# Kernel optimization log

Measured on AMD Instinct MI355X. Metric: run time of the kernel, lower is better.

The kernel has to match this reference:

```python
import jax, jax.numpy as jnp
import numpy as np

WORD_THRES = 0.2
COS_EPS = 1e-8
NEG_INF = -1e9


def setup_inputs() -> dict:
    key = jax.random.key(0)
    k1, k2, k3, k4 = jax.random.split(key, 4)
    B, L, V, E, A = 1024, 256, 50000, 300, 30
    inputs = jax.random.randint(k1, (B, L), 0, V)            # token ids, 0 == pad
    w_emb = jax.random.normal(k2, (V, E), dtype=jnp.float32) * 0.1
    a_emb = jax.random.normal(k3, (A, E), dtype=jnp.float32)
    a_weight = jax.random.uniform(k4, (A,), dtype=jnp.float32)
    return {"inputs": inputs, "w_emb": w_emb, "a_emb": a_emb, "a_weight": a_weight}


def reference(inputs, w_emb, a_emb, a_weight):
    # inputs: [B, L] int ids; w_emb: [V, E]; a_emb: [A, E]; a_weight: [A]
    inputs_len = (inputs != 0).sum(axis=1).astype(jnp.float32)      # [B]
    x_wrd = w_emb[inputs]                                            # [B, L, E]

    # cosine similarity between each aspect and each word (torch semantics:
    # dot / (max(||a||, eps) * max(||x||, eps)))
    a_norm = jnp.maximum(jnp.linalg.norm(a_emb, axis=-1), COS_EPS)   # [A]
    x_norm = jnp.maximum(jnp.linalg.norm(x_wrd, axis=-1), COS_EPS)   # [B, L]
    dot = jnp.einsum("ae,ble->abl", a_emb, x_wrd)                    # [A, B, L]
    sim = dot / (a_norm[:, None, None] * x_norm[None, :, :])

    # Threshold(word_thres, 0): x if x > thres else 0, then scale by aspect weight
    sim = jnp.where(sim > WORD_THRES, sim, 0.0) * a_weight[:, None, None]

    # centroid score: relu(sim).max over aspects, summed over seq, length-normalized
    centroid = jnp.maximum(sim, 0.0).max(axis=0)                     # [B, L]
    centroid_score = centroid.sum(axis=1) / (inputs_len + 1e-5)      # [B]

    # attention: mask exact zeros to -1e9, max over aspects, softmax over seq
    sim_m = jnp.where(sim == 0.0, NEG_INF, sim)
    scores = sim_m.max(axis=0)                                       # [B, L]
    a = jax.nn.softmax(scores, axis=1)                               # [B, L]

    z = jnp.einsum("bl,ble->be", a, x_wrd)                           # [B, E]
    enc_out = z * (centroid_score > 1e-4).astype(z.dtype)[:, None]
    return enc_out, a, centroid_score
```

## Files before the change

kernel.cpp:

```cpp
#include <hip/hip_runtime.h>
#include <math.h>

#define BB 1024
#define LL 256
#define VV 50000
#define EE 300
#define AA 30
#define WORD_THRES 0.2f
#define COS_EPS_F 1e-8f
#define NEG_INF_F -1e9f
#define RECHECK_DELTA 1e-3f

typedef __attribute__((ext_vector_type(8))) short bf16x8;
typedef __attribute__((ext_vector_type(4))) float f32x4;

#define MFMA16(a, b, c) __builtin_amdgcn_mfma_f32_16x16x32_bf16((a), (b), (c), 0, 0, 0)

__device__ __forceinline__ unsigned pack_hi(float a, float b) {
    return (__float_as_uint(a) >> 16) | (__float_as_uint(b) & 0xFFFF0000u);
}
__device__ __forceinline__ float hi_part(float a) {
    return __uint_as_float(__float_as_uint(a) & 0xFFFF0000u);
}
__device__ __forceinline__ void cvt_hilo(const float4 f0, const float4 f1,
                                         uint4& uh, uint4& ul) {
    uh.x = pack_hi(f0.x, f0.y);
    uh.y = pack_hi(f0.z, f0.w);
    uh.z = pack_hi(f1.x, f1.y);
    uh.w = pack_hi(f1.z, f1.w);
    const float l0 = f0.x - hi_part(f0.x), l1 = f0.y - hi_part(f0.y);
    const float l2 = f0.z - hi_part(f0.z), l3 = f0.w - hi_part(f0.w);
    const float l4 = f1.x - hi_part(f1.x), l5 = f1.y - hi_part(f1.y);
    const float l6 = f1.z - hi_part(f1.z), l7 = f1.w - hi_part(f1.w);
    ul.x = pack_hi(l0, l1);
    ul.y = pack_hi(l2, l3);
    ul.z = pack_hi(l4, l5);
    ul.w = pack_hi(l6, l7);
}

__global__ void __launch_bounds__(256) cent_kernel(
    const float* __restrict__ w_emb,
    const float* __restrict__ a_emb,
    const float* __restrict__ a_weight,
    float* __restrict__ cent)
{
    __shared__ uint4 s_bfrag[40 * 64];
    __shared__ float s_scale[32];
    __shared__ float s_aw[32];

    const int t = threadIdx.x;
    const int l = t & 63;
    const int w = t >> 6;
    const int m = l & 15;
    const int kg = l >> 4;

    {
        const int a = t >> 3, j = t & 7;
        if (a < AA) {
            const float4* a4 = (const float4*)a_emb + a * 75;
            float n2a = 0.f;
            for (int c = j; c < 75; c += 8) {
                const float4 x = a4[c];
                n2a += x.x * x.x + x.y * x.y + x.z * x.z + x.w * x.w;
            }
            n2a += __shfl_xor(n2a, 1);
            n2a += __shfl_xor(n2a, 2);
            n2a += __shfl_xor(n2a, 4);
            if (j == 0) {
                s_scale[a] = 1.f / fmaxf(sqrtf(n2a), COS_EPS_F);
                s_aw[a] = a_weight[a];
            }
        }
        if (t == 30 || t == 31) { s_scale[t] = 0.f; s_aw[t] = 0.f; }
    }

    for (int ks = w; ks < 10; ks += 4) {
        const int kb = kg * 8 + 32 * ks;
#pragma unroll
        for (int tt = 0; tt < 2; ++tt) {
            const int col = tt * 16 + m;
            float4 f0 = {0.f, 0.f, 0.f, 0.f}, f1 = {0.f, 0.f, 0.f, 0.f};
            if (col < AA) {
                const float* ap = a_emb + col * EE;
                if (kb <= 296) f0 = *(const float4*)(ap + kb);
                if (kb <= 292) f1 = *(const float4*)(ap + kb + 4);
            }
            uint4 uh, ul;
            cvt_hilo(f0, f1, uh, ul);
            s_bfrag[(ks * 4 + tt * 2 + 0) * 64 + l] = uh;
            s_bfrag[(ks * 4 + tt * 2 + 1) * 64 + l] = ul;
        }
    }
    __syncthreads();

    const int vbase = blockIdx.x * 64 + w * 16;
    const int v = vbase + m;
    const float* __restrict__ rowp = w_emb + (size_t)((v < VV) ? v : 0) * EE;

    f32x4 acc0 = {0.f, 0.f, 0.f, 0.f};
    f32x4 acc1 = {0.f, 0.f, 0.f, 0.f};
    float n2 = 0.f;
    const uint4* __restrict__ bp0 = s_bfrag + l;

#pragma unroll 3
    for (int ks = 0; ks < 9; ++ks) {
        const int kb = kg * 8 + 32 * ks;
        const float4 f0 = *(const float4*)(rowp + kb);
        const float4 f1 = *(const float4*)(rowp + kb + 4);
        n2 = fmaf(f0.x, f0.x, fmaf(f0.y, f0.y, fmaf(f0.z, f0.z, fmaf(f0.w, f0.w, n2))));
        n2 = fmaf(f1.x, f1.x, fmaf(f1.y, f1.y, fmaf(f1.z, f1.z, fmaf(f1.w, f1.w, n2))));
        uint4 uh, ul;
        cvt_hilo(f0, f1, uh, ul);
        const bf16x8 ah = __builtin_bit_cast(bf16x8, uh);
        const bf16x8 al = __builtin_bit_cast(bf16x8, ul);
        const uint4* bp = bp0 + ks * 256;
        const bf16x8 bh0 = __builtin_bit_cast(bf16x8, bp[0]);
        const bf16x8 bl0 = __builtin_bit_cast(bf16x8, bp[64]);
        const bf16x8 bh1 = __builtin_bit_cast(bf16x8, bp[128]);
        const bf16x8 bl1 = __builtin_bit_cast(bf16x8, bp[192]);
        acc0 = MFMA16(ah, bh0, acc0);
        acc1 = MFMA16(ah, bh1, acc1);
        acc0 = MFMA16(ah, bl0, acc0);
        acc1 = MFMA16(ah, bl1, acc1);
        acc0 = MFMA16(al, bh0, acc0);
        acc1 = MFMA16(al, bh1, acc1);
    }
    {
        const int kb = kg * 8 + 288;
        float4 f0 = {0.f, 0.f, 0.f, 0.f}, f1 = {0.f, 0.f, 0.f, 0.f};
        if (kb <= 296) f0 = *(const float4*)(rowp + kb);
        if (kb <= 292) f1 = *(const float4*)(rowp + kb + 4);
        n2 = fmaf(f0.x, f0.x, fmaf(f0.y, f0.y, fmaf(f0.z, f0.z, fmaf(f0.w, f0.w, n2))));
        n2 = fmaf(f1.x, f1.x, fmaf(f1.y, f1.y, fmaf(f1.z, f1.z, fmaf(f1.w, f1.w, n2))));
        uint4 uh, ul;
        cvt_hilo(f0, f1, uh, ul);
        const bf16x8 ah = __builtin_bit_cast(bf16x8, uh);
        const bf16x8 al = __builtin_bit_cast(bf16x8, ul);
        const uint4* bp = bp0 + 9 * 256;
        const bf16x8 bh0 = __builtin_bit_cast(bf16x8, bp[0]);
        const bf16x8 bl0 = __builtin_bit_cast(bf16x8, bp[64]);
        const bf16x8 bh1 = __builtin_bit_cast(bf16x8, bp[128]);
        const bf16x8 bl1 = __builtin_bit_cast(bf16x8, bp[192]);
        acc0 = MFMA16(ah, bh0, acc0);
        acc1 = MFMA16(ah, bh1, acc1);
        acc0 = MFMA16(ah, bl0, acc0);
        acc1 = MFMA16(ah, bl1, acc1);
        acc0 = MFMA16(al, bh0, acc0);
        acc1 = MFMA16(al, bh1, acc1);
    }

    n2 += __shfl_xor(n2, 16);
    n2 += __shfl_xor(n2, 32);

    const float sc0 = s_scale[m], aw0 = s_aw[m];
    const float sc1 = s_scale[16 + m], aw1 = s_aw[16 + m];
    const bool col1ok = (16 + m) < AA;
    float mx[4];
#pragma unroll
    for (int j = 0; j < 4; ++j) {
        const int r = kg * 4 + j;
        const float n2r = __int_as_float(
            __builtin_amdgcn_ds_bpermute(r << 2, __float_as_int(n2)));
        const float inv_x = 1.f / fmaxf(sqrtf(n2r), COS_EPS_F);
        float c0 = acc0[j] * sc0 * inv_x;
        float c1 = acc1[j] * sc1 * inv_x;
        if (fabsf(c0 - WORD_THRES) < RECHECK_DELTA) {
            const int rr = vbase + r;
            const float* wr = w_emb + (size_t)((rr < VV) ? rr : 0) * EE;
            const float* ar = a_emb + m * EE;
            float d = 0.f;
            for (int k = 0; k < EE; ++k) d = fmaf(wr[k], ar[k], d);
            c0 = d * sc0 * inv_x;
        }
        if (col1ok && fabsf(c1 - WORD_THRES) < RECHECK_DELTA) {
            const int rr = vbase + r;
            const float* wr = w_emb + (size_t)((rr < VV) ? rr : 0) * EE;
            const float* ar = a_emb + (16 + m) * EE;
            float d = 0.f;
            for (int k = 0; k < EE; ++k) d = fmaf(wr[k], ar[k], d);
            c1 = d * sc1 * inv_x;
        }
        float mj = fmaxf((c0 > WORD_THRES) ? c0 * aw0 : 0.f,
                         (c1 > WORD_THRES) ? c1 * aw1 : 0.f);
        mj = fmaxf(mj, __shfl_xor(mj, 1));
        mj = fmaxf(mj, __shfl_xor(mj, 2));
        mj = fmaxf(mj, __shfl_xor(mj, 4));
        mj = fmaxf(mj, __shfl_xor(mj, 8));
        mx[j] = mj;
    }
    if (m == 0 && vbase < VV) {
        const float4 o = {mx[0], mx[1], mx[2], mx[3]};
        *(float4*)(cent + vbase + kg * 4) = o;
    }
}

__global__ void __launch_bounds__(256) row_kernel(
    const int* __restrict__ inputs,
    const float* __restrict__ w_emb,
    const float* __restrict__ cent,
    float* __restrict__ out)
{
    const int b = blockIdx.x;
    const int t = threadIdx.x;
    const int wid = t >> 6, lane = t & 63;

    __shared__ float pA[4], pB[4], pC[4], pD[4];
    __shared__ int s_nact;
    __shared__ int s_act_id[LL];
    __shared__ float s_act_w[LL];

    const int id = inputs[b * LL + t];
    const float c = cent[id];
    const float score = (c > 0.f) ? c : NEG_INF_F;
    const float cnt = (id != 0) ? 1.f : 0.f;
    if (t == 0) s_nact = 0;

    float s1 = c, s2 = cnt, s3 = score;
#pragma unroll
    for (int o = 32; o > 0; o >>= 1) {
        s1 += __shfl_down(s1, o);
        s2 += __shfl_down(s2, o);
        s3 = fmaxf(s3, __shfl_down(s3, o));
    }
    if (lane == 0) { pA[wid] = s1; pB[wid] = s2; pC[wid] = s3; }
    __syncthreads();

    const float sum_c = pA[0] + pA[1] + pA[2] + pA[3];
    const float len   = pB[0] + pB[1] + pB[2] + pB[3];
    const float mx    = fmaxf(fmaxf(pC[0], pC[1]), fmaxf(pC[2], pC[3]));

    const float p = expf(score - mx);
    float s4 = p;
#pragma unroll
    for (int o = 32; o > 0; o >>= 1) s4 += __shfl_down(s4, o);
    if (lane == 0) pD[wid] = s4;
    __syncthreads();
    const float sum_p = pD[0] + pD[1] + pD[2] + pD[3];

    const float a_l = p / sum_p;
    const float cs = sum_c / (len + 1e-5f);
    const float gate = (cs > 1e-4f) ? 1.f : 0.f;

    out[BB * EE + b * LL + t] = a_l;
    if (t == 0) out[BB * EE + BB * LL + b] = cs;

    if (score > -1e8f) {
        const int i = atomicAdd(&s_nact, 1);
        s_act_id[i] = id;
        s_act_w[i] = a_l;
    }
    __syncthreads();
    const int n = s_nact;

    if (t < EE / 4) {
        float4 acc = {0.f, 0.f, 0.f, 0.f};
        for (int i = 0; i < n; ++i) {
            const float wgt = s_act_w[i];
            const float4 r = *(const float4*)(w_emb + (size_t)s_act_id[i] * EE + 4 * t);
            acc.x += wgt * r.x; acc.y += wgt * r.y;
            acc.z += wgt * r.z; acc.w += wgt * r.w;
        }
        acc.x *= gate; acc.y *= gate; acc.z *= gate; acc.w *= gate;
        *(float4*)(out + b * EE + 4 * t) = acc;
    }
}

extern "C" void kernel_launch(void* const* d_in, const int* in_sizes, int n_in,
                              void* d_out, int out_size, void* d_ws, size_t ws_size,
                              hipStream_t stream) {
    const int* inputs = (const int*)d_in[0];
    const float* w_emb = (const float*)d_in[1];
    const float* a_emb = (const float*)d_in[2];
    const float* a_weight = (const float*)d_in[3];
    float* out = (float*)d_out;
    float* cent = (float*)d_ws;

    cent_kernel<<<(VV + 63) / 64, 256, 0, stream>>>(w_emb, a_emb, a_weight, cent);
    row_kernel<<<BB, 256, 0, stream>>>(inputs, w_emb, cent, out);
}
```

Before: 114.4 us.

## Prefetch embedding rows in registers and map one row per wavefront

In cent_kernel the K loop is fully unrolled into 10 steps. Five float4 pairs are prefetched into registers ahead of use, which hides global load latency, and the clamped loads replace the guarded tail step. row_kernel now gives each batch row to one wavefront, four rows per block, so all reductions are wave shuffles with no block barriers, and all 64 lanes take part in the weighted gather instead of 75 threads per block. The recheck delta is also tightened. This adds register pressure and leaves one launch of 256 blocks for the row stage.

```diff
diff --git a/kernel.cpp b/kernel.cpp
--- a/kernel.cpp
+++ b/kernel.cpp
@@ -9,7 +9,7 @@
 #define WORD_THRES 0.2f
 #define COS_EPS_F 1e-8f
 #define NEG_INF_F -1e9f
-#define RECHECK_DELTA 1e-3f
+#define RECHECK_DELTA 2e-4f
 
 typedef __attribute__((ext_vector_type(8))) short bf16x8;
 typedef __attribute__((ext_vector_type(4))) float f32x4;
@@ -36,6 +36,14 @@
     ul.y = pack_hi(l2, l3);
     ul.z = pack_hi(l4, l5);
     ul.w = pack_hi(l6, l7);
+}
+
+__device__ __forceinline__ void ld_pair(const float* __restrict__ rowp, int kb,
+                                        float4& a, float4& b) {
+    const int k0 = (kb > 296) ? 296 : kb;
+    const int k1 = (kb + 4 > 296) ? 296 : (kb + 4);
+    a = *(const float4*)(rowp + k0);
+    b = *(const float4*)(rowp + k1);
 }
 
 __global__ void __launch_bounds__(256) cent_kernel(
@@ -102,41 +110,29 @@
     float n2 = 0.f;
     const uint4* __restrict__ bp0 = s_bfrag + l;
 
-#pragma unroll 3
-    for (int ks = 0; ks < 9; ++ks) {
-        const int kb = kg * 8 + 32 * ks;
-        const float4 f0 = *(const float4*)(rowp + kb);
-        const float4 f1 = *(const float4*)(rowp + kb + 4);
+    float4 pa[5], pb[5];
+#pragma unroll
+    for (int i = 0; i < 5; ++i)
+        ld_pair(rowp, kg * 8 + 32 * i, pa[i], pb[i]);
+
+#pragma unroll
+    for (int i = 0; i < 10; ++i) {
+        const int s = i % 5;
+        float4 f0 = pa[s], f1 = pb[s];
+        if (i < 5)
+            ld_pair(rowp, kg * 8 + 32 * (i + 5), pa[s], pb[s]);
+        if (i == 9) {
+            const float4 z = {0.f, 0.f, 0.f, 0.f};
+            if (kg >= 2) f0 = z;
+            if (kg >= 1) f1 = z;
+        }
         n2 = fmaf(f0.x, f0.x, fmaf(f0.y, f0.y, fmaf(f0.z, f0.z, fmaf(f0.w, f0.w, n2))));
         n2 = fmaf(f1.x, f1.x, fmaf(f1.y, f1.y, fmaf(f1.z, f1.z, fmaf(f1.w, f1.w, n2))));
         uint4 uh, ul;
         cvt_hilo(f0, f1, uh, ul);
         const bf16x8 ah = __builtin_bit_cast(bf16x8, uh);
         const bf16x8 al = __builtin_bit_cast(bf16x8, ul);
-        const uint4* bp = bp0 + ks * 256;
-        const bf16x8 bh0 = __builtin_bit_cast(bf16x8, bp[0]);
-        const bf16x8 bl0 = __builtin_bit_cast(bf16x8, bp[64]);
-        const bf16x8 bh1 = __builtin_bit_cast(bf16x8, bp[128]);
-        const bf16x8 bl1 = __builtin_bit_cast(bf16x8, bp[192]);
-        acc0 = MFMA16(ah, bh0, acc0);
-        acc1 = MFMA16(ah, bh1, acc1);
-        acc0 = MFMA16(ah, bl0, acc0);
-        acc1 = MFMA16(ah, bl1, acc1);
-        acc0 = MFMA16(al, bh0, acc0);
-        acc1 = MFMA16(al, bh1, acc1);
-    }
-    {
-        const int kb = kg * 8 + 288;
-        float4 f0 = {0.f, 0.f, 0.f, 0.f}, f1 = {0.f, 0.f, 0.f, 0.f};
-        if (kb <= 296) f0 = *(const float4*)(rowp + kb);
-        if (kb <= 292) f1 = *(const float4*)(rowp + kb + 4);
-        n2 = fmaf(f0.x, f0.x, fmaf(f0.y, f0.y, fmaf(f0.z, f0.z, fmaf(f0.w, f0.w, n2))));
-        n2 = fmaf(f1.x, f1.x, fmaf(f1.y, f1.y, fmaf(f1.z, f1.z, fmaf(f1.w, f1.w, n2))));
-        uint4 uh, ul;
-        cvt_hilo(f0, f1, uh, ul);
-        const bf16x8 ah = __builtin_bit_cast(bf16x8, uh);
-        const bf16x8 al = __builtin_bit_cast(bf16x8, ul);
-        const uint4* bp = bp0 + 9 * 256;
+        const uint4* bp = bp0 + i * 256;
         const bf16x8 bh0 = __builtin_bit_cast(bf16x8, bp[0]);
         const bf16x8 bl0 = __builtin_bit_cast(bf16x8, bp[64]);
         const bf16x8 bh1 = __builtin_bit_cast(bf16x8, bp[128]);
@@ -200,68 +196,80 @@
     const float* __restrict__ cent,
     float* __restrict__ out)
 {
-    const int b = blockIdx.x;
-    const int t = threadIdx.x;
-    const int wid = t >> 6, lane = t & 63;
-
-    __shared__ float pA[4], pB[4], pC[4], pD[4];
-    __shared__ int s_nact;
-    __shared__ int s_act_id[LL];
-    __shared__ float s_act_w[LL];
-
-    const int id = inputs[b * LL + t];
-    const float c = cent[id];
-    const float score = (c > 0.f) ? c : NEG_INF_F;
-    const float cnt = (id != 0) ? 1.f : 0.f;
-    if (t == 0) s_nact = 0;
-
-    float s1 = c, s2 = cnt, s3 = score;
-#pragma unroll
-    for (int o = 32; o > 0; o >>= 1) {
-        s1 += __shfl_down(s1, o);
-        s2 += __shfl_down(s2, o);
-        s3 = fmaxf(s3, __shfl_down(s3, o));
-    }
-    if (lane == 0) { pA[wid] = s1; pB[wid] = s2; pC[wid] = s3; }
+    const int w = threadIdx.x >> 6;
+    const int lane = threadIdx.x & 63;
+    const int b = blockIdx.x * 4 + w;
+
+    __shared__ int s_id[4][LL];
+    __shared__ float s_w[4][LL];
+    __shared__ int s_n[4];
+
+    if (lane == 0) s_n[w] = 0;
+
+    const int4 id4 = *(const int4*)(inputs + b * LL + lane * 4);
+    const float c0 = cent[id4.x];
+    const float c1 = cent[id4.y];
+    const float c2 = cent[id4.z];
+    const float c3 = cent[id4.w];
+    const float sc0 = (c0 > 0.f) ? c0 : NEG_INF_F;
+    const float sc1 = (c1 > 0.f) ? c1 : NEG_INF_F;
+    const float sc2 = (c2 > 0.f) ? c2 : NEG_INF_F;
+    const float sc3 = (c3 > 0.f) ? c3 : NEG_INF_F;
+
+    float s1 = c0 + c1 + c2 + c3;
+    float s2 = (id4.x != 0 ? 1.f : 0.f) + (id4.y != 0 ? 1.f : 0.f) +
+               (id4.z != 0 ? 1.f : 0.f) + (id4.w != 0 ? 1.f : 0.f);
+    float s3 = fmaxf(fmaxf(sc0, sc1), fmaxf(sc2, sc3));
+#pragma unroll
+    for (int o = 1; o < 64; o <<= 1) {
+        s1 += __shfl_xor(s1, o);
+        s2 += __shfl_xor(s2, o);
+        s3 = fmaxf(s3, __shfl_xor(s3, o));
+    }
+    const float mx = s3;
+
+    const float p0 = expf(sc0 - mx);
+    const float p1 = expf(sc1 - mx);
+    const float p2 = expf(sc2 - mx);
+    const float p3 = expf(sc3 - mx);
+    float s4 = p0 + p1 + p2 + p3;
+#pragma unroll
+    for (int o = 1; o < 64; o <<= 1) s4 += __shfl_xor(s4, o);
+
+    const float rinv = 1.f / s4;
+    const float4 av = {p0 * rinv, p1 * rinv, p2 * rinv, p3 * rinv};
+    *(float4*)(out + BB * EE + b * LL + lane * 4) = av;
+
+    const float cs = s1 / (s2 + 1e-5f);
+    const float gate = (cs > 1e-4f) ? 1.f : 0.f;
+    if (lane == 0) out[BB * EE + BB * LL + b] = cs;
+
+    if (sc0 > -1e8f) { const int i = atomicAdd(&s_n[w], 1); s_id[w][i] = id4.x; s_w[w][i] = av.x; }
+    if (sc1 > -1e8f) { const int i = atomicAdd(&s_n[w], 1); s_id[w][i] = id4.y; s_w[w][i] = av.y; }
+    if (sc2 > -1e8f) { const int i = atomicAdd(&s_n[w], 1); s_id[w][i] = id4.z; s_w[w][i] = av.z; }
+    if (sc3 > -1e8f) { const int i = atomicAdd(&s_n[w], 1); s_id[w][i] = id4.w; s_w[w][i] = av.w; }
     __syncthreads();
-
-    const float sum_c = pA[0] + pA[1] + pA[2] + pA[3];
-    const float len   = pB[0] + pB[1] + pB[2] + pB[3];
-    const float mx    = fmaxf(fmaxf(pC[0], pC[1]), fmaxf(pC[2], pC[3]));
-
-    const float p = expf(score - mx);
-    float s4 = p;
-#pragma unroll
-    for (int o = 32; o > 0; o >>= 1) s4 += __shfl_down(s4, o);
-    if (lane == 0) pD[wid] = s4;
-    __syncthreads();
-    const float sum_p = pD[0] + pD[1] + pD[2] + pD[3];
-
-    const float a_l = p / sum_p;
-    const float cs = sum_c / (len + 1e-5f);
-    const float gate = (cs > 1e-4f) ? 1.f : 0.f;
-
-    out[BB * EE + b * LL + t] = a_l;
-    if (t == 0) out[BB * EE + BB * LL + b] = cs;
-
-    if (score > -1e8f) {
-        const int i = atomicAdd(&s_nact, 1);
-        s_act_id[i] = id;
-        s_act_w[i] = a_l;
-    }
-    __syncthreads();
-    const int n = s_nact;
-
-    if (t < EE / 4) {
-        float4 acc = {0.f, 0.f, 0.f, 0.f};
-        for (int i = 0; i < n; ++i) {
-            const float wgt = s_act_w[i];
-            const float4 r = *(const float4*)(w_emb + (size_t)s_act_id[i] * EE + 4 * t);
-            acc.x += wgt * r.x; acc.y += wgt * r.y;
-            acc.z += wgt * r.z; acc.w += wgt * r.w;
-        }
-        acc.x *= gate; acc.y *= gate; acc.z *= gate; acc.w *= gate;
-        *(float4*)(out + b * EE + 4 * t) = acc;
+    const int n = s_n[w];
+
+    float4 accA = {0.f, 0.f, 0.f, 0.f};
+    float4 accB = {0.f, 0.f, 0.f, 0.f};
+    for (int i = 0; i < n; ++i) {
+        const float wgt = s_w[w][i];
+        const float4* rp = (const float4*)(w_emb + (size_t)s_id[w][i] * EE);
+        const float4 ra = rp[lane];
+        accA.x += wgt * ra.x; accA.y += wgt * ra.y;
+        accA.z += wgt * ra.z; accA.w += wgt * ra.w;
+        if (lane < 11) {
+            const float4 rb = rp[64 + lane];
+            accB.x += wgt * rb.x; accB.y += wgt * rb.y;
+            accB.z += wgt * rb.z; accB.w += wgt * rb.w;
+        }
+    }
+    accA.x *= gate; accA.y *= gate; accA.z *= gate; accA.w *= gate;
+    *(float4*)(out + b * EE + 4 * lane) = accA;
+    if (lane < 11) {
+        accB.x *= gate; accB.y *= gate; accB.z *= gate; accB.w *= gate;
+        *(float4*)(out + b * EE + 256 + 4 * lane) = accB;
     }
 }
 
@@ -276,5 +284,5 @@
     float* cent = (float*)d_ws;
 
     cent_kernel<<<(VV + 63) / 64, 256, 0, stream>>>(w_emb, a_emb, a_weight, cent);
-    row_kernel<<<BB, 256, 0, stream>>>(inputs, w_emb, cent, out);
-}
+    row_kernel<<<BB / 4, 256, 0, stream>>>(inputs, w_emb, cent, out);
+}
```

Result: faster. 111.6 us (median of 2 runs) (-2.4%).
